# Performance work log

Hardware: AMD Instinct MI355X
Metric: run time of the kernel (lower is better)

## Reference

```python
import jax, jax.numpy as jnp
import numpy as np

MASK_FILL = -100.0


def setup_inputs() -> dict:
    key = jax.random.key(0)
    k1, k2, k3, k4 = jax.random.split(key, 4)
    B, S1, S2, D_IN, D_OUT = 8, 2048, 2048, 1024, 1024
    input1 = jax.random.normal(k1, (B, S1, D_IN), dtype=jnp.float32)
    input2 = jax.random.normal(k2, (B, S2, D_OUT), dtype=jnp.float32)
    input_mask = jax.random.randint(k3, (B, S1), 0, 2) > 0  # bool [B,S1]
    # kaiming_uniform-ish init scale for weight [out_features, in_features]
    bound = 1.0 / np.sqrt(D_IN)
    weight = jax.random.uniform(k4, (D_OUT, D_IN), dtype=jnp.float32,
                                minval=-bound, maxval=bound)
    return {"input1": input1, "input2": input2,
            "input_mask": input_mask, "weight": weight}


def reference(input1, input2, input_mask, weight):
    # out1 = F.linear(input1, weight): [B,S1,in] @ [in,out] -> [B,S1,out]
    out1 = jnp.einsum('bsd,od->bso', input1, weight)
    # scores: [B,S1,out] x [B,S2,out]^T -> [B,S1,S2]
    scores = jnp.einsum('bso,bto->bst', out1, input2)
    # out2[~input_mask] = -100 : mask is [B,S1], zeroes whole rows of scores
    scores = jnp.where(input_mask[:, :, None], scores, MASK_FILL)
    # softmax over S1 (dim=1), then attn^T @ input1 -> [B,S2,in]
    attn = jax.nn.softmax(scores, axis=1)
    satt = jnp.einsum('bst,bsd->btd', attn, input1)
    return satt
```

## Files before the change

### kernel.cpp

```cpp
#include <hip/hip_runtime.h>


typedef short s16x8 __attribute__((ext_vector_type(8)));
typedef float f32x4 __attribute__((ext_vector_type(4)));
typedef unsigned short u16;
typedef unsigned short u16x8 __attribute__((ext_vector_type(8)));
typedef _Float16 f16x8v __attribute__((ext_vector_type(8)));

#define B_ 8
#define S1_ 2048
#define S2_ 2048
#define D_ 1024
#define LDET 2064

__device__ __forceinline__ float b2f(u16 u) {
  return __uint_as_float(((unsigned int)u) << 16);
}
__device__ __forceinline__ u16 f2b(float f) {
  unsigned int x = __float_as_uint(f);
  return (u16)((x + 0x7FFFu + ((x >> 16) & 1u)) >> 16);
}
__device__ __forceinline__ u16 f2h(float f) {
  _Float16 h = (_Float16)f;
  return __builtin_bit_cast(u16, h);
}
__device__ __forceinline__ float h2f(u16 u) {
  return (float)__builtin_bit_cast(_Float16, u);
}
__device__ __forceinline__ void gload16(const void* g, void* l) {
  __builtin_amdgcn_global_load_lds(
      (const __attribute__((address_space(1))) unsigned int*)g,
      (__attribute__((address_space(3))) unsigned int*)l, 16, 0, 0);
}

template <bool F16>
__device__ __forceinline__ f32x4 mfma16(s16x8 a, s16x8 b, f32x4 c) {
  if constexpr (F16)
    return __builtin_amdgcn_mfma_f32_16x16x32_f16(
        __builtin_bit_cast(f16x8v, a), __builtin_bit_cast(f16x8v, b), c, 0, 0,
        0);
  else
    return __builtin_amdgcn_mfma_f32_16x16x32_bf16(a, b, c, 0, 0, 0);
}


__global__ __launch_bounds__(256) void split_h_kernel(
    const float* __restrict__ in, u16* __restrict__ h, int n4) {
  int i = blockIdx.x * 256 + threadIdx.x;
  if (i >= n4) return;
  f32x4 v = ((const f32x4*)in)[i];
  ushort4 o;
  o.x = f2h(v[0]);
  o.y = f2h(v[1]);
  o.z = f2h(v[2]);
  o.w = f2h(v[3]);
  ((ushort4*)h)[i] = o;
}

__global__ __launch_bounds__(256) void zero_kernel(float* __restrict__ p,
                                                   int n) {
  int i = blockIdx.x * 256 + threadIdx.x;
  if (i < n) p[i] = 0.f;
}

__global__ __launch_bounds__(256) void compact_kernel(
    const int* __restrict__ mask, int* __restrict__ sidx,
    int* __restrict__ cnt, int* __restrict__ kr) {
  const int b = blockIdx.x;
  const int* mb = mask + (long)b * S1_;
  int* sb = sidx + (long)b * S1_;
  const int t = threadIdx.x;
  const int lane = t & 63, w = t >> 6;
  __shared__ int wsum[4];
  int loc[8], c = 0;
#pragma unroll
  for (int j = 0; j < 8; ++j) {
    loc[j] = (mb[t * 8 + j] != 0);
    c += loc[j];
  }
  int inc = c;
  for (int off = 1; off < 64; off <<= 1) {
    int v = __shfl_up(inc, off, 64);
    if (lane >= off) inc += v;
  }
  if (lane == 63) wsum[w] = inc;
  __syncthreads();
  int woff = 0;
#pragma unroll
  for (int i = 0; i < 4; ++i)
    if (i < w) woff += wsum[i];
  int pos = woff + inc - c;
#pragma unroll
  for (int j = 0; j < 8; ++j)
    if (loc[j]) sb[pos++] = t * 8 + j;
  if (t == 255) {
    int tot = woff + inc;
    cnt[b] = tot;
    int r = (tot + 127) & ~127;
    if (r < 256) r = 256;
    kr[b] = r;
  }
}

__global__ __launch_bounds__(256) void gather_split_kernel(
    const float* __restrict__ in, const int* __restrict__ sidx,
    const int* __restrict__ cnt, const int* __restrict__ kr,
    u16* __restrict__ outh) {
  const int b = blockIdx.y;
  const int r = blockIdx.x;
  if (r >= kr[b]) return;
  u16* orow = outh + ((size_t)b * S1_ + r) * D_;
  const int t = threadIdx.x;
  if (r < cnt[b]) {
    const int src = sidx[(size_t)b * S1_ + r];
    f32x4 v = *(const f32x4*)(in + ((size_t)b * S1_ + src) * D_ + t * 4);
    ushort4 o;
    o.x = f2h(v[0]);
    o.y = f2h(v[1]);
    o.z = f2h(v[2]);
    o.w = f2h(v[3]);
    *(ushort4*)(orow + t * 4) = o;
  } else {
    ushort4 z = {0, 0, 0, 0};
    *(ushort4*)(orow + t * 4) = z;
  }
}

template <int NSEG, int MODE, bool F16, bool EXITM, bool DYNK>
__global__ __launch_bounds__(512, 2) void gemm8(
    const u16* __restrict__ A0, const u16* __restrict__ A1,
    const u16* __restrict__ A2, const u16* __restrict__ B0,
    const u16* __restrict__ B1, const u16* __restrict__ B2,
    void* __restrict__ Cp, u16* __restrict__ C2, int K, int lda, int ldb,
    int ldc, long sA, long sB, long sC, const int* __restrict__ cntArr,
    const int* __restrict__ krArr, float* __restrict__ lvec, int lvecStride) {
  __shared__ __align__(16) u16 Abuf0[8192];
  __shared__ __align__(16) u16 Abuf1[8192];
  __shared__ __align__(16) u16 Abuf2[8192];
  __shared__ __align__(16) u16 Abuf3[8192];
  __shared__ __align__(16) u16 Bbuf0[8192];
  __shared__ __align__(16) u16 Bbuf1[8192];
  __shared__ __align__(16) u16 Bbuf2[8192];
  __shared__ __align__(16) u16 Bbuf3[8192];

  const int gx = gridDim.x, gy = gridDim.y;
  int flat = blockIdx.x + gx * (blockIdx.y + gy * blockIdx.z);
  const int total = gx * gy * (int)gridDim.z;
  const int cpx = total >> 3;
  flat = (flat & 7) * cpx + (flat >> 3);
  const int bx = flat % gx;
  const int rem0 = flat / gx;
  const int by = rem0 % gy;
  const int bz = rem0 / gy;

  if constexpr (EXITM) {
    if (by * 256 >= krArr[bz]) return;
  }
  if constexpr (MODE == 1) {
    if (bx * 256 >= krArr[bz]) return;
  }

  const int tid = threadIdx.x;
  const int lane = tid & 63;
  const int wid = tid >> 6;
  const int wr = wid >> 2;
  const int wn = wid & 3;

  const int Keff = DYNK ? krArr[bz] : K;
  const int tps = Keff >> 5;
  const int NT = NSEG * tps;

  const int srow = tid >> 2;
  const int kch = (tid & 3) ^ ((srow >> 1) & 3);
  const long aRow1 = (long)(by * 256 + srow) * lda + kch * 8;
  const long aRow2 = (long)(by * 256 + srow + 128) * lda + kch * 8;
  const long bRow1 = (long)(bx * 256 + srow) * ldb + kch * 8;
  const long bRow2 = (long)(bx * 256 + srow + 128) * ldb + kch * 8;

  const u16* aBase0 = A0 + (long)bz * sA;
  const u16* bBase0 = B0 + (long)bz * sB;
  const u16* aBase1 = (NSEG > 1) ? A1 + (long)bz * sA : aBase0;
  const u16* bBase1 = (NSEG > 1) ? B1 + (long)bz * sB : bBase0;
  const u16* aBase2 = (NSEG > 2) ? A2 + (long)bz * sA : aBase0;
  const u16* bBase2 = (NSEG > 2) ? B2 + (long)bz * sB : bBase0;

  const int lr = lane & 15;
  const int kg = lane >> 4;
  const int arow0 = wr * 128 + lr;
  const int aOffU = arow0 * 32 + (kg ^ ((arow0 >> 1) & 3)) * 8;
  const int brow0 = wn * 64 + lr;
  const int bOffU = brow0 * 32 + (kg ^ ((brow0 >> 1) & 3)) * 8;

  const f32x4 z4 = {0.f, 0.f, 0.f, 0.f};
  f32x4 acc[8][4];
#pragma unroll
  for (int i = 0; i < 8; ++i)
#pragma unroll
    for (int j = 0; j < 4; ++j) acc[i][j] = z4;

  int s_rem = 0, s_seg = 0;
  const u16* aS = aBase0;
  const u16* bS = bBase0;

#define STAGE_AB(DA_, DB_)                                                   \
  {                                                                          \
    gload16(aS + aRow1 + s_rem * 32, &DA_[wid * 512]);                       \
    gload16(aS + aRow2 + s_rem * 32, &DA_[wid * 512 + 4096]);                \
    gload16(bS + bRow1 + s_rem * 32, &DB_[wid * 512]);                       \
    gload16(bS + bRow2 + s_rem * 32, &DB_[wid * 512 + 4096]);                \
    if (++s_rem == tps) {                                                    \
      s_rem = 0;                                                             \
      ++s_seg;                                                               \
      aS = (s_seg == 1) ? aBase1 : aBase2;                                   \
      bS = (s_seg == 1) ? bBase1 : bBase2;                                   \
    }                                                                        \
  }

  STAGE_AB(Abuf0, Bbuf0);
  STAGE_AB(Abuf1, Bbuf1);
  STAGE_AB(Abuf2, Bbuf2);
  asm volatile("s_waitcnt vmcnt(8)" ::: "memory");
  __builtin_amdgcn_s_barrier();

#define ITER(AS_, BS_, DA_, DB_, VM_, STG_)                                  \
  {                                                                          \
    s16x8 a0[4], a1[4], bfr[4];                                              \
    _Pragma("unroll") for (int m_ = 0; m_ < 4; ++m_) a0[m_] =                \
        *(const s16x8*)&AS_[aOffU + m_ * 512];                               \
    _Pragma("unroll") for (int n_ = 0; n_ < 4; ++n_) bfr[n_] =               \
        *(const s16x8*)&BS_[bOffU + n_ * 512];                               \
    _Pragma("unroll") for (int m_ = 0; m_ < 4; ++m_) a1[m_] =                \
        *(const s16x8*)&AS_[aOffU + (m_ + 4) * 512];                         \
    if (STG_) {                                                              \
      gload16(aS + aRow1 + s_rem * 32, &DA_[wid * 512]);                     \
      gload16(aS + aRow2 + s_rem * 32, &DA_[wid * 512 + 4096]);              \
    }                                                                        \
    asm volatile("" ::: "memory");                                           \
    __builtin_amdgcn_s_barrier();                                            \
    __builtin_amdgcn_sched_barrier(0);                                       \
    __builtin_amdgcn_s_setprio(1);                                           \
    _Pragma("unroll") for (int m_ = 0; m_ < 4; ++m_)                         \
        _Pragma("unroll") for (int n_ = 0; n_ < 4; ++n_) acc[m_][n_] =       \
            mfma16<F16>(a0[m_], bfr[n_], acc[m_][n_]);                       \
    __builtin_amdgcn_s_setprio(0);                                           \
    if (STG_) {                                                              \
      gload16(bS + bRow1 + s_rem * 32, &DB_[wid * 512]);                     \
      gload16(bS + bRow2 + s_rem * 32, &DB_[wid * 512 + 4096]);              \
      if (++s_rem == tps) {                                                  \
        s_rem = 0;                                                           \
        ++s_seg;                                                             \
        aS = (s_seg == 1) ? aBase1 : aBase2;                                 \
        bS = (s_seg == 1) ? bBase1 : bBase2;                                 \
      }                                                                      \
    }                                                                        \
    asm volatile("s_waitcnt " VM_ ::: "memory");                             \
    __builtin_amdgcn_s_barrier();                                            \
    __builtin_amdgcn_sched_barrier(0);                                       \
    __builtin_amdgcn_s_setprio(1);                                           \
    _Pragma("unroll") for (int m_ = 0; m_ < 4; ++m_)                         \
        _Pragma("unroll") for (int n_ = 0; n_ < 4; ++n_) acc[m_ + 4][n_] =   \
            mfma16<F16>(a1[m_], bfr[n_], acc[m_ + 4][n_]);                   \
    __builtin_amdgcn_s_setprio(0);                                           \
  }

  for (int t = 0; t < NT - 4; t += 4) {
    ITER(Abuf0, Bbuf0, Abuf3, Bbuf3, "vmcnt(8)", true);
    ITER(Abuf1, Bbuf1, Abuf0, Bbuf0, "vmcnt(8)", true);
    ITER(Abuf2, Bbuf2, Abuf1, Bbuf1, "vmcnt(8)", true);
    ITER(Abuf3, Bbuf3, Abuf2, Bbuf2, "vmcnt(8)", true);
  }
  ITER(Abuf0, Bbuf0, Abuf3, Bbuf3, "vmcnt(8)", true);
  ITER(Abuf1, Bbuf1, Abuf0, Bbuf0, "vmcnt(4)", false);
  ITER(Abuf2, Bbuf2, Abuf1, Bbuf1, "vmcnt(0)", false);
  ITER(Abuf3, Bbuf3, Abuf2, Bbuf2, "vmcnt(0)", false);

#undef ITER
#undef STAGE_AB

  const int row0 = by * 256 + wr * 128 + kg * 4;
  const int col0 = bx * 256 + wn * 64 + lr;

  if (MODE == 0) {
    u16* Ch = (u16*)Cp + (long)bz * sC;
    u16* Cl = C2 + (long)bz * sC;
#pragma unroll
    for (int m = 0; m < 8; ++m)
#pragma unroll
      for (int n = 0; n < 4; ++n)
#pragma unroll
        for (int r = 0; r < 4; ++r) {
          float v = acc[m][n][r];
          long idx = (long)(row0 + m * 16 + r) * ldc + (col0 + n * 16);
          if (F16) {
            u16 h = f2h(v);
            Ch[idx] = h;
            Cl[idx] = f2h(v - h2f(h));
          } else {
            u16 h = f2b(v);
            Ch[idx] = h;
            Cl[idx] = f2b(v - b2f(h));
          }
        }
  } else if (MODE == 1) {
    u16* Cb = (u16*)Cp + (long)bz * sC;
    float* lvout = lvec + (long)bz * lvecStride;
    const int cn = cntArr[bz];
    int mcol[4];
#pragma unroll
    for (int n = 0; n < 4; ++n) mcol[n] = (col0 + n * 16) < cn;
#pragma unroll
    for (int m = 0; m < 8; ++m)
#pragma unroll
      for (int r = 0; r < 4; ++r) {
        float rv = 0.f;
#pragma unroll
        for (int n = 0; n < 4; ++n) {
          float v = acc[m][n][r];
          v = mcol[n] ? __expf(v - 100.0f) : 0.0f;
          Cb[(long)(row0 + m * 16 + r) * ldc + (col0 + n * 16)] = f2b(v);
          rv += v;
        }
        rv += __shfl_xor(rv, 1, 16);
        rv += __shfl_xor(rv, 2, 16);
        rv += __shfl_xor(rv, 4, 16);
        rv += __shfl_xor(rv, 8, 16);
        if (lr == 0) atomicAdd(&lvout[row0 + m * 16 + r], rv);
      }
  } else {
    float* Cb = (float*)Cp + (long)bz * sC;
    const float* lb = lvec + (long)bz * lvecStride;
#pragma unroll
    for (int m = 0; m < 8; ++m) {
      float sc[4];
#pragma unroll
      for (int r = 0; r < 4; ++r) {
        float dv = lb[row0 + m * 16 + r];
        sc[r] = (dv > 0.0f) ? 1.0f / dv : 0.0f;
      }
#pragma unroll
      for (int n = 0; n < 4; ++n)
#pragma unroll
        for (int r = 0; r < 4; ++r)
          Cb[(long)(row0 + m * 16 + r) * ldc + (col0 + n * 16)] =
              acc[m][n][r] * sc[r];
    }
  }
}


__device__ __forceinline__ void split8(const float* __restrict__ g, s16x8& h,
                                       s16x8& l) {
  f32x4 a = *(const f32x4*)g;
  f32x4 b = *(const f32x4*)(g + 4);
#pragma unroll
  for (int j = 0; j < 8; ++j) {
    float x = (j < 4) ? a[j] : b[j - 4];
    u16 hu = f2b(x);
    h[j] = (short)hu;
    l[j] = (short)f2b(x - b2f(hu));
  }
}

template <int MODE>
__global__ __launch_bounds__(256, 2) void gemm_k(
    const void* __restrict__ Ap, const void* __restrict__ Bp,
    const u16* __restrict__ Blo, void* __restrict__ Cp, u16* __restrict__ C2,
    int K, int ldc, long sA, long sB, long sC, const int* __restrict__ mask,
    int maskStride, const float* __restrict__ lvec, int lvecStride) {
  constexpr bool TRI = (MODE != 2);
  __shared__ s16x8 AsH[512];
  __shared__ s16x8 BsH[512];
  __shared__ s16x8 AsL[TRI ? 512 : 1];
  __shared__ s16x8 BsL[TRI ? 512 : 1];

  const int z = blockIdx.z;
  const int tid = threadIdx.x;
  const int lane = tid & 63;
  const int wid = tid >> 6;

  const f32x4 z4 = {0.f, 0.f, 0.f, 0.f};
  f32x4 acc[4][4];
#pragma unroll
  for (int i = 0; i < 4; ++i)
#pragma unroll
    for (int j = 0; j < 4; ++j) acc[i][j] = z4;

  const int wm = (wid & 1) * 64;
  const int wn = (wid >> 1) * 64;
  const int lrow = lane & 15;
  const int kofs = (lane >> 4) * 8;
  const int srow = tid >> 1;
  const int shalf = (tid & 1) * 16;
  const int lidx = (srow * 32 + shalf) >> 3;

  const u16* AsHu = (const u16*)AsH;
  const u16* BsHu = (const u16*)BsH;
  const u16* AsLu = (const u16*)AsL;
  const u16* BsLu = (const u16*)BsL;

  for (int k0 = 0; k0 < K; k0 += 32) {
    if (MODE == 2) {
      const u16* Ab = (const u16*)Ap + z * sA + (long)blockIdx.y * 128 * K;
      const u16* Bb = (const u16*)Bp + z * sB + (long)blockIdx.x * 128 * K;
      const u16* ga = Ab + (long)srow * K + k0 + shalf;
      const u16* gb = Bb + (long)srow * K + k0 + shalf;
      AsH[lidx] = *(const s16x8*)ga;
      AsH[lidx + 1] = *(const s16x8*)(ga + 8);
      BsH[lidx] = *(const s16x8*)gb;
      BsH[lidx + 1] = *(const s16x8*)(gb + 8);
    } else {
      const float* Ab = (const float*)Ap + z * sA + (long)blockIdx.y * 128 * K;
      const float* ga = Ab + (long)srow * K + k0 + shalf;
      split8(ga, AsH[lidx], AsL[lidx]);
      split8(ga + 8, AsH[lidx + 1], AsL[lidx + 1]);
      if (MODE == 0) {
        const float* Bb = (const float*)Bp + z * sB + (long)blockIdx.x * 128 * K;
        const float* gb = Bb + (long)srow * K + k0 + shalf;
        split8(gb, BsH[lidx], BsL[lidx]);
        split8(gb + 8, BsH[lidx + 1], BsL[lidx + 1]);
      } else {
        const u16* Bh = (const u16*)Bp + z * sB + (long)blockIdx.x * 128 * K;
        const u16* Bl = Blo + z * sB + (long)blockIdx.x * 128 * K;
        const u16* gh = Bh + (long)srow * K + k0 + shalf;
        const u16* gl = Bl + (long)srow * K + k0 + shalf;
        BsH[lidx] = *(const s16x8*)gh;
        BsH[lidx + 1] = *(const s16x8*)(gh + 8);
        BsL[lidx] = *(const s16x8*)gl;
        BsL[lidx + 1] = *(const s16x8*)(gl + 8);
      }
    }
    __syncthreads();
    s16x8 ah[4], bh[4], al[4], bl[4];
#pragma unroll
    for (int t = 0; t < 4; ++t) {
      ah[t] = *(const s16x8*)&AsHu[(wm + t * 16 + lrow) * 32 + kofs];
      bh[t] = *(const s16x8*)&BsHu[(wn + t * 16 + lrow) * 32 + kofs];
      if (TRI) {
        al[t] = *(const s16x8*)&AsLu[(wm + t * 16 + lrow) * 32 + kofs];
        bl[t] = *(const s16x8*)&BsLu[(wn + t * 16 + lrow) * 32 + kofs];
      }
    }
#pragma unroll
    for (int i = 0; i < 4; ++i)
#pragma unroll
      for (int j = 0; j < 4; ++j) {
        acc[i][j] = __builtin_amdgcn_mfma_f32_16x16x32_bf16(ah[i], bh[j],
                                                            acc[i][j], 0, 0, 0);
        if (TRI) {
          acc[i][j] = __builtin_amdgcn_mfma_f32_16x16x32_bf16(
              al[i], bh[j], acc[i][j], 0, 0, 0);
          acc[i][j] = __builtin_amdgcn_mfma_f32_16x16x32_bf16(
              ah[i], bl[j], acc[i][j], 0, 0, 0);
        }
      }
    __syncthreads();
  }

  const int row0 = blockIdx.y * 128 + wm + (lane >> 4) * 4;
  const int col0 = blockIdx.x * 128 + wn + lrow;

  if (MODE == 0) {
    u16* Ch = (u16*)Cp;
#pragma unroll
    for (int i = 0; i < 4; ++i)
#pragma unroll
      for (int j = 0; j < 4; ++j)
#pragma unroll
        for (int r = 0; r < 4; ++r) {
          float v = acc[i][j][r];
          long idx = (long)(row0 + i * 16 + r) * ldc + (col0 + j * 16);
          u16 h = f2b(v);
          Ch[idx] = h;
          C2[idx] = f2b(v - b2f(h));
        }
  } else if (MODE == 1) {
    u16* Cb = (u16*)Cp + z * sC;
    const int* mb = mask + (long)z * maskStride;
    int mcol[4];
#pragma unroll
    for (int j = 0; j < 4; ++j) mcol[j] = mb[col0 + j * 16];
#pragma unroll
    for (int i = 0; i < 4; ++i)
#pragma unroll
      for (int j = 0; j < 4; ++j)
#pragma unroll
        for (int r = 0; r < 4; ++r) {
          float v = acc[i][j][r];
          v = mcol[j] ? __expf(v - 100.0f) : 0.0f;
          Cb[(long)(row0 + i * 16 + r) * ldc + (col0 + j * 16)] = f2b(v);
        }
  } else {
    float* Cb = (float*)Cp + z * sC;
    const float* lb = lvec + (long)z * lvecStride;
    float scale[4][4];
#pragma unroll
    for (int i = 0; i < 4; ++i)
#pragma unroll
      for (int r = 0; r < 4; ++r) {
        float dv = lb[row0 + i * 16 + r];
        scale[i][r] = (dv > 0.0f) ? 1.0f / dv : 0.0f;
      }
#pragma unroll
    for (int i = 0; i < 4; ++i)
#pragma unroll
      for (int j = 0; j < 4; ++j)
#pragma unroll
        for (int r = 0; r < 4; ++r)
          Cb[(long)(row0 + i * 16 + r) * ldc + (col0 + j * 16)] =
              acc[i][j][r] * scale[i][r];
  }
}


__global__ __launch_bounds__(256) void rowsum_kernel(const u16* __restrict__ E,
                                                     float* __restrict__ l) {
  const int row = blockIdx.x * 4 + (threadIdx.x >> 6);
  const int lane = threadIdx.x & 63;
  const u16* p = E + (size_t)row * S1_;
  float s = 0.f;
#pragma unroll
  for (int j = 0; j < 4; ++j) {
    u16x8 v = *(const u16x8*)(p + (j * 64 + lane) * 8);
#pragma unroll
    for (int k = 0; k < 8; ++k) s += b2f(v[k]);
  }
#pragma unroll
  for (int off = 32; off; off >>= 1) s += __shfl_down(s, off, 64);
  if (lane == 0) l[row] = s;
}

__global__ __launch_bounds__(256) void transposeC_kernel(
    const float* __restrict__ in, const int* __restrict__ sidx,
    const int* __restrict__ cnt, const int* __restrict__ kr,
    u16* __restrict__ out) {
  __shared__ u16 tile[64][66];
  const int b = blockIdx.z;
  const int s0 = blockIdx.x * 64;
  if (s0 >= kr[b]) return;
  const int cn = cnt[b];
  const int* sx = sidx + (long)b * S1_;
  const float* ib = in + (size_t)b * S1_ * D_;
  u16* ob = out + (size_t)b * D_ * LDET;
  const int d0 = blockIdx.y * 64;
  const int t = threadIdx.x;
  const int tr = t >> 4;
  const int tc = (t & 15) * 4;
#pragma unroll
  for (int i = 0; i < 4; ++i) {
    int row = tr + i * 16;
    int j = s0 + row;
    if (j < cn) {
      f32x4 v = *(const f32x4*)(ib + (size_t)sx[j] * D_ + d0 + tc);
      tile[row][tc + 0] = f2b(v[0]);
      tile[row][tc + 1] = f2b(v[1]);
      tile[row][tc + 2] = f2b(v[2]);
      tile[row][tc + 3] = f2b(v[3]);
    } else {
      tile[row][tc + 0] = 0;
      tile[row][tc + 1] = 0;
      tile[row][tc + 2] = 0;
      tile[row][tc + 3] = 0;
    }
  }
  __syncthreads();
#pragma unroll
  for (int i = 0; i < 4; ++i) {
    int drow = tr + i * 16;
    ushort4 w;
    w.x = tile[tc + 0][drow];
    w.y = tile[tc + 1][drow];
    w.z = tile[tc + 2][drow];
    w.w = tile[tc + 3][drow];
    *(ushort4*)(ob + (size_t)(d0 + drow) * LDET + s0 + tc) = w;
  }
}

__global__ __launch_bounds__(256) void transpose_kernel(
    const float* __restrict__ in, u16* __restrict__ out) {
  __shared__ u16 tile[64][66];
  const int b = blockIdx.z;
  const float* ib = in + (size_t)b * S1_ * D_;
  u16* ob = out + (size_t)b * D_ * S1_;
  const int s0 = blockIdx.x * 64;
  const int d0 = blockIdx.y * 64;
  const int t = threadIdx.x;
  const int tr = t >> 4;
  const int tc = (t & 15) * 4;
#pragma unroll
  for (int i = 0; i < 4; ++i) {
    int row = tr + i * 16;
    f32x4 v = *(const f32x4*)(ib + (size_t)(s0 + row) * D_ + d0 + tc);
    tile[row][tc + 0] = f2b(v[0]);
    tile[row][tc + 1] = f2b(v[1]);
    tile[row][tc + 2] = f2b(v[2]);
    tile[row][tc + 3] = f2b(v[3]);
  }
  __syncthreads();
#pragma unroll
  for (int i = 0; i < 4; ++i) {
    int drow = tr + i * 16;
    ushort4 w;
    w.x = tile[tc + 0][drow];
    w.y = tile[tc + 1][drow];
    w.z = tile[tc + 2][drow];
    w.w = tile[tc + 3][drow];
    *(ushort4*)(ob + (size_t)(d0 + drow) * S1_ + s0 + tc) = w;
  }
}


extern "C" void kernel_launch(void* const* d_in, const int* in_sizes, int n_in,
                              void* d_out, int out_size, void* d_ws,
                              size_t ws_size, hipStream_t stream) {
  const float* in1 = (const float*)d_in[0];
  const float* in2 = (const float*)d_in[1];
  const int* mask = (const int*)d_in[2];
  const float* W = (const float*)d_in[3];
  float* out = (float*)d_out;
  char* ws = (char*)d_ws;
  const size_t MB = 1024 * 1024;
  dim3 blk(256);
  dim3 blk512(512);

  const size_t FULL_WS = 196 * MB + 64 * 1024;
  if (ws_size >= FULL_WS) {
    u16* in1C_h = (u16*)(ws + 0);
    u16* in1TC = (u16*)(ws + 0);
    u16* in2_h = (u16*)(ws + 33816576UL);
    u16* W_h = (u16*)(ws + 67371008UL);
    u16* ET = (u16*)(ws + 69468160UL);
    u16* out1C_h = (u16*)(ws + 137101312UL);
    u16* out1C_l = (u16*)(ws + 170655744UL);
    float* lv = (float*)(ws + 204210176UL);
    int* sidx = (int*)(ws + 204275712UL);
    int* cnt = (int*)(ws + 204341248UL);
    int* kr = cnt + 8;

    split_h_kernel<<<dim3(16384), blk, 0, stream>>>(in2, in2_h,
                                                    B_ * S2_ * D_ / 4);
    split_h_kernel<<<dim3(1024), blk, 0, stream>>>(W, W_h, D_ * D_ / 4);
    zero_kernel<<<dim3(128), blk, 0, stream>>>(lv, 32768);
    compact_kernel<<<dim3(B_), blk, 0, stream>>>(mask, sidx, cnt, kr);
    gather_split_kernel<<<dim3(S1_, B_), blk, 0, stream>>>(in1, sidx, cnt, kr,
                                                           in1C_h);

    gemm8<1, 0, true, true, false><<<dim3(4, 8, B_), blk512, 0, stream>>>(
        in1C_h, in1C_h, in1C_h, W_h, W_h, W_h, out1C_h, out1C_l, D_, D_, D_,
        D_, (long)S1_ * D_, 0L, (long)S1_ * D_, cnt, kr, nullptr, 0);

    gemm8<2, 1, true, false, false><<<dim3(8, 8, B_), blk512, 0, stream>>>(
        in2_h, in2_h, in2_h, out1C_h, out1C_l, out1C_l, ET, nullptr, D_, D_,
        D_, LDET, (long)S2_ * D_, (long)S1_ * D_, (long)S1_ * LDET, cnt, kr,
        lv, S2_);

    transposeC_kernel<<<dim3(S1_ / 64, D_ / 64, B_), blk, 0, stream>>>(
        in1, sidx, cnt, kr, in1TC);

    gemm8<1, 2, false, false, true><<<dim3(4, 8, B_), blk512, 0, stream>>>(
        ET, ET, ET, in1TC, in1TC, in1TC, out, nullptr, 0, LDET, LDET, D_,
        (long)S1_ * LDET, (long)D_ * LDET, (long)S2_ * D_, cnt, kr, lv, S2_);
  } else {
    u16* out1_hi = (u16*)ws;
    u16* out1_lo = (u16*)(ws + 32 * MB);
    u16* ET = (u16*)(ws + 64 * MB);
    float* lv = (float*)(ws + 128 * MB);
    u16* in1T = out1_hi;

    gemm_k<0><<<dim3(8, 128, 1), blk, 0, stream>>>(
        in1, W, nullptr, out1_hi, out1_lo, D_, D_, 0, 0, 0, nullptr, 0,
        nullptr, 0);
    gemm_k<1><<<dim3(16, 16, B_), blk, 0, stream>>>(
        in2, out1_hi, out1_lo, ET, nullptr, D_, S1_, (long)S2_ * D_,
        (long)S1_ * D_, (long)S2_ * S1_, mask, S1_, nullptr, 0);
    rowsum_kernel<<<dim3(B_ * S2_ / 4), blk, 0, stream>>>(ET, lv);
    transpose_kernel<<<dim3(S1_ / 64, D_ / 64, B_), blk, 0, stream>>>(in1, in1T);
    gemm_k<2><<<dim3(8, 16, B_), blk, 0, stream>>>(
        ET, in1T, nullptr, out, nullptr, S1_, D_, (long)S2_ * S1_,
        (long)D_ * S1_, (long)S2_ * D_, nullptr, 0, lv, S2_);
  }
}
```

Measured before the change: 392.7 us.

## Shrink GEMM tiles to 128x128 with 256-thread blocks and simpler pipeline

The three gemm8 launches now use 128x128 output tiles computed by 4 waves of 256 threads instead of 256x256 tiles on 8 waves of 512 threads. LDS buffers are halved, and each wave's accumulator drops from 8x4 to 4x4 MFMA tiles. The inner iteration is restructured so all A/B staging loads are issued together, followed by one MFMA block and one barrier, replacing the previous split half-iteration schedule. Smaller tiles give more blocks and finer masked early-exit granularity, at the cost of lower arithmetic intensity per loaded byte and more global/LDS traffic.

```diff
diff --git a/kernel.cpp b/kernel.cpp
--- a/kernel.cpp
+++ b/kernel.cpp
@@ -127,21 +127,21 @@
 }
 
 template <int NSEG, int MODE, bool F16, bool EXITM, bool DYNK>
-__global__ __launch_bounds__(512, 2) void gemm8(
+__global__ __launch_bounds__(256) void gemm8(
     const u16* __restrict__ A0, const u16* __restrict__ A1,
     const u16* __restrict__ A2, const u16* __restrict__ B0,
     const u16* __restrict__ B1, const u16* __restrict__ B2,
     void* __restrict__ Cp, u16* __restrict__ C2, int K, int lda, int ldb,
     int ldc, long sA, long sB, long sC, const int* __restrict__ cntArr,
     const int* __restrict__ krArr, float* __restrict__ lvec, int lvecStride) {
-  __shared__ __align__(16) u16 Abuf0[8192];
-  __shared__ __align__(16) u16 Abuf1[8192];
-  __shared__ __align__(16) u16 Abuf2[8192];
-  __shared__ __align__(16) u16 Abuf3[8192];
-  __shared__ __align__(16) u16 Bbuf0[8192];
-  __shared__ __align__(16) u16 Bbuf1[8192];
-  __shared__ __align__(16) u16 Bbuf2[8192];
-  __shared__ __align__(16) u16 Bbuf3[8192];
+  __shared__ __align__(16) u16 Abuf0[4096];
+  __shared__ __align__(16) u16 Abuf1[4096];
+  __shared__ __align__(16) u16 Abuf2[4096];
+  __shared__ __align__(16) u16 Abuf3[4096];
+  __shared__ __align__(16) u16 Bbuf0[4096];
+  __shared__ __align__(16) u16 Bbuf1[4096];
+  __shared__ __align__(16) u16 Bbuf2[4096];
+  __shared__ __align__(16) u16 Bbuf3[4096];
 
   const int gx = gridDim.x, gy = gridDim.y;
   int flat = blockIdx.x + gx * (blockIdx.y + gy * blockIdx.z);
@@ -154,17 +154,17 @@
   const int bz = rem0 / gy;
 
   if constexpr (EXITM) {
-    if (by * 256 >= krArr[bz]) return;
+    if (by * 128 >= krArr[bz]) return;
   }
   if constexpr (MODE == 1) {
-    if (bx * 256 >= krArr[bz]) return;
+    if (bx * 128 >= krArr[bz]) return;
   }
 
   const int tid = threadIdx.x;
   const int lane = tid & 63;
   const int wid = tid >> 6;
-  const int wr = wid >> 2;
-  const int wn = wid & 3;
+  const int wr = wid >> 1;
+  const int wn = wid & 1;
 
   const int Keff = DYNK ? krArr[bz] : K;
   const int tps = Keff >> 5;
@@ -172,10 +172,10 @@
 
   const int srow = tid >> 2;
   const int kch = (tid & 3) ^ ((srow >> 1) & 3);
-  const long aRow1 = (long)(by * 256 + srow) * lda + kch * 8;
-  const long aRow2 = (long)(by * 256 + srow + 128) * lda + kch * 8;
-  const long bRow1 = (long)(bx * 256 + srow) * ldb + kch * 8;
-  const long bRow2 = (long)(bx * 256 + srow + 128) * ldb + kch * 8;
+  const long aRowA = (long)(by * 128 + srow) * lda + kch * 8;
+  const long aRowB = (long)(by * 128 + 64 + srow) * lda + kch * 8;
+  const long bRowA = (long)(bx * 128 + srow) * ldb + kch * 8;
+  const long bRowB = (long)(bx * 128 + 64 + srow) * ldb + kch * 8;
 
   const u16* aBase0 = A0 + (long)bz * sA;
   const u16* bBase0 = B0 + (long)bz * sB;
@@ -186,15 +186,15 @@
 
   const int lr = lane & 15;
   const int kg = lane >> 4;
-  const int arow0 = wr * 128 + lr;
+  const int arow0 = wr * 64 + lr;
   const int aOffU = arow0 * 32 + (kg ^ ((arow0 >> 1) & 3)) * 8;
   const int brow0 = wn * 64 + lr;
   const int bOffU = brow0 * 32 + (kg ^ ((brow0 >> 1) & 3)) * 8;
 
   const f32x4 z4 = {0.f, 0.f, 0.f, 0.f};
-  f32x4 acc[8][4];
-#pragma unroll
-  for (int i = 0; i < 8; ++i)
+  f32x4 acc[4][4];
+#pragma unroll
+  for (int i = 0; i < 4; ++i)
 #pragma unroll
     for (int j = 0; j < 4; ++j) acc[i][j] = z4;
 
@@ -204,10 +204,10 @@
 
 #define STAGE_AB(DA_, DB_)                                                   \
   {                                                                          \
-    gload16(aS + aRow1 + s_rem * 32, &DA_[wid * 512]);                       \
-    gload16(aS + aRow2 + s_rem * 32, &DA_[wid * 512 + 4096]);                \
-    gload16(bS + bRow1 + s_rem * 32, &DB_[wid * 512]);                       \
-    gload16(bS + bRow2 + s_rem * 32, &DB_[wid * 512 + 4096]);                \
+    gload16(aS + aRowA + s_rem * 32, &DA_[wid * 512]);                       \
+    gload16(aS + aRowB + s_rem * 32, &DA_[wid * 512 + 2048]);                \
+    gload16(bS + bRowA + s_rem * 32, &DB_[wid * 512]);                       \
+    gload16(bS + bRowB + s_rem * 32, &DB_[wid * 512 + 2048]);                \
     if (++s_rem == tps) {                                                    \
       s_rem = 0;                                                             \
       ++s_seg;                                                               \
@@ -222,69 +222,50 @@
   asm volatile("s_waitcnt vmcnt(8)" ::: "memory");
   __builtin_amdgcn_s_barrier();
 
-#define ITER(AS_, BS_, DA_, DB_, VM_, STG_)                                  \
+#define ITER(AS_, BS_, DA_, DB_, VM_, STG_, BAR_)                            \
   {                                                                          \
-    s16x8 a0[4], a1[4], bfr[4];                                              \
-    _Pragma("unroll") for (int m_ = 0; m_ < 4; ++m_) a0[m_] =                \
+    s16x8 af[4], bf[4];                                                      \
+    _Pragma("unroll") for (int m_ = 0; m_ < 4; ++m_) af[m_] =                \
         *(const s16x8*)&AS_[aOffU + m_ * 512];                               \
-    _Pragma("unroll") for (int n_ = 0; n_ < 4; ++n_) bfr[n_] =               \
+    _Pragma("unroll") for (int n_ = 0; n_ < 4; ++n_) bf[n_] =                \
         *(const s16x8*)&BS_[bOffU + n_ * 512];                               \
-    _Pragma("unroll") for (int m_ = 0; m_ < 4; ++m_) a1[m_] =                \
-        *(const s16x8*)&AS_[aOffU + (m_ + 4) * 512];                         \
-    if (STG_) {                                                              \
-      gload16(aS + aRow1 + s_rem * 32, &DA_[wid * 512]);                     \
-      gload16(aS + aRow2 + s_rem * 32, &DA_[wid * 512 + 4096]);              \
-    }                                                                        \
-    asm volatile("" ::: "memory");                                           \
-    __builtin_amdgcn_s_barrier();                                            \
-    __builtin_amdgcn_sched_barrier(0);                                       \
+    if (STG_) STAGE_AB(DA_, DB_);                                            \
     __builtin_amdgcn_s_setprio(1);                                           \
     _Pragma("unroll") for (int m_ = 0; m_ < 4; ++m_)                         \
         _Pragma("unroll") for (int n_ = 0; n_ < 4; ++n_) acc[m_][n_] =       \
-            mfma16<F16>(a0[m_], bfr[n_], acc[m_][n_]);                       \
+            mfma16<F16>(af[m_], bf[n_], acc[m_][n_]);                        \
     __builtin_amdgcn_s_setprio(0);                                           \
-    if (STG_) {                                                              \
-      gload16(bS + bRow1 + s_rem * 32, &DB_[wid * 512]);                     \
-      gload16(bS + bRow2 + s_rem * 32, &DB_[wid * 512 + 4096]);              \
-      if (++s_rem == tps) {                                                  \
-        s_rem = 0;                                                           \
-        ++s_seg;                                                             \
-        aS = (s_seg == 1) ? aBase1 : aBase2;                                 \
-        bS = (s_seg == 1) ? bBase1 : bBase2;                                 \
-      }                                                                      \
+    asm volatile("s_waitcnt " VM_ ::: "memory");                             \
+    if (BAR_) {                                                              \
+      asm volatile("" ::: "memory");                                         \
+      __builtin_amdgcn_s_barrier();                                          \
+      asm volatile("" ::: "memory");                                         \
     }                                                                        \
-    asm volatile("s_waitcnt " VM_ ::: "memory");                             \
-    __builtin_amdgcn_s_barrier();                                            \
-    __builtin_amdgcn_sched_barrier(0);                                       \
-    __builtin_amdgcn_s_setprio(1);                                           \
-    _Pragma("unroll") for (int m_ = 0; m_ < 4; ++m_)                         \
-        _Pragma("unroll") for (int n_ = 0; n_ < 4; ++n_) acc[m_ + 4][n_] =   \
-            mfma16<F16>(a1[m_], bfr[n_], acc[m_ + 4][n_]);                   \
-    __builtin_amdgcn_s_setprio(0);                                           \
-  }
-
-  for (int t = 0; t < NT - 4; t += 4) {
-    ITER(Abuf0, Bbuf0, Abuf3, Bbuf3, "vmcnt(8)", true);
-    ITER(Abuf1, Bbuf1, Abuf0, Bbuf0, "vmcnt(8)", true);
-    ITER(Abuf2, Bbuf2, Abuf1, Bbuf1, "vmcnt(8)", true);
-    ITER(Abuf3, Bbuf3, Abuf2, Bbuf2, "vmcnt(8)", true);
-  }
-  ITER(Abuf0, Bbuf0, Abuf3, Bbuf3, "vmcnt(8)", true);
-  ITER(Abuf1, Bbuf1, Abuf0, Bbuf0, "vmcnt(4)", false);
-  ITER(Abuf2, Bbuf2, Abuf1, Bbuf1, "vmcnt(0)", false);
-  ITER(Abuf3, Bbuf3, Abuf2, Bbuf2, "vmcnt(0)", false);
+  }
+
+  const int G = (NT >> 2) - 1;
+  for (int g = 0; g < G; ++g) {
+    ITER(Abuf0, Bbuf0, Abuf3, Bbuf3, "vmcnt(8)", true, true);
+    ITER(Abuf1, Bbuf1, Abuf0, Bbuf0, "vmcnt(8)", true, true);
+    ITER(Abuf2, Bbuf2, Abuf1, Bbuf1, "vmcnt(8)", true, true);
+    ITER(Abuf3, Bbuf3, Abuf2, Bbuf2, "vmcnt(8)", true, true);
+  }
+  ITER(Abuf0, Bbuf0, Abuf3, Bbuf3, "vmcnt(8)", true, true);
+  ITER(Abuf1, Bbuf1, Abuf0, Bbuf0, "vmcnt(4)", false, true);
+  ITER(Abuf2, Bbuf2, Abuf1, Bbuf1, "vmcnt(0)", false, true);
+  ITER(Abuf3, Bbuf3, Abuf2, Bbuf2, "vmcnt(0)", false, false);
 
 #undef ITER
 #undef STAGE_AB
 
-  const int row0 = by * 256 + wr * 128 + kg * 4;
-  const int col0 = bx * 256 + wn * 64 + lr;
+  const int row0 = by * 128 + wr * 64 + kg * 4;
+  const int col0 = bx * 128 + wn * 64 + lr;
 
   if (MODE == 0) {
     u16* Ch = (u16*)Cp + (long)bz * sC;
     u16* Cl = C2 + (long)bz * sC;
 #pragma unroll
-    for (int m = 0; m < 8; ++m)
+    for (int m = 0; m < 4; ++m)
 #pragma unroll
       for (int n = 0; n < 4; ++n)
 #pragma unroll
@@ -309,7 +290,7 @@
 #pragma unroll
     for (int n = 0; n < 4; ++n) mcol[n] = (col0 + n * 16) < cn;
 #pragma unroll
-    for (int m = 0; m < 8; ++m)
+    for (int m = 0; m < 4; ++m)
 #pragma unroll
       for (int r = 0; r < 4; ++r) {
         float rv = 0.f;
@@ -330,7 +311,7 @@
     float* Cb = (float*)Cp + (long)bz * sC;
     const float* lb = lvec + (long)bz * lvecStride;
 #pragma unroll
-    for (int m = 0; m < 8; ++m) {
+    for (int m = 0; m < 4; ++m) {
       float sc[4];
 #pragma unroll
       for (int r = 0; r < 4; ++r) {
@@ -620,7 +601,6 @@
   char* ws = (char*)d_ws;
   const size_t MB = 1024 * 1024;
   dim3 blk(256);
-  dim3 blk512(512);
 
   const size_t FULL_WS = 196 * MB + 64 * 1024;
   if (ws_size >= FULL_WS) {
@@ -644,11 +624,11 @@
     gather_split_kernel<<<dim3(S1_, B_), blk, 0, stream>>>(in1, sidx, cnt, kr,
                                                            in1C_h);
 
-    gemm8<1, 0, true, true, false><<<dim3(4, 8, B_), blk512, 0, stream>>>(
+    gemm8<1, 0, true, true, false><<<dim3(8, 16, B_), blk, 0, stream>>>(
         in1C_h, in1C_h, in1C_h, W_h, W_h, W_h, out1C_h, out1C_l, D_, D_, D_,
         D_, (long)S1_ * D_, 0L, (long)S1_ * D_, cnt, kr, nullptr, 0);
 
-    gemm8<2, 1, true, false, false><<<dim3(8, 8, B_), blk512, 0, stream>>>(
+    gemm8<2, 1, true, false, false><<<dim3(16, 16, B_), blk, 0, stream>>>(
         in2_h, in2_h, in2_h, out1C_h, out1C_l, out1C_l, ET, nullptr, D_, D_,
         D_, LDET, (long)S2_ * D_, (long)S1_ * D_, (long)S1_ * LDET, cnt, kr,
         lv, S2_);
@@ -656,7 +636,7 @@
     transposeC_kernel<<<dim3(S1_ / 64, D_ / 64, B_), blk, 0, stream>>>(
         in1, sidx, cnt, kr, in1TC);
 
-    gemm8<1, 2, false, false, true><<<dim3(4, 8, B_), blk512, 0, stream>>>(
+    gemm8<1, 2, false, false, true><<<dim3(8, 16, B_), blk, 0, stream>>>(
         ET, ET, ET, in1TC, in1TC, in1TC, out, nullptr, 0, LDET, LDET, D_,
         (long)S1_ * LDET, (long)D_ * LDET, (long)S2_ * D_, cnt, kr, lv, S2_);
   } else {
```

Measured after the change: 392.9 us. About the same (+0.0%).
